# Performance work log

Measured on AMD Instinct MI355X. Metric: run time of the kernel, lower is better.

## Reference

```python
import jax, jax.numpy as jnp
import numpy as np

B, N, D = 4, 2048, 1024


def setup_inputs() -> dict:
    key = jax.random.key(0)
    ks = jax.random.split(key, 9)
    x = jax.random.normal(ks[0], (B, N, D), dtype=jnp.float32)
    # causal mask: True = masked (set to -inf), per dot_product_attention semantics
    mask = jnp.triu(jnp.ones((N, N), dtype=bool), k=1)
    mask = jnp.broadcast_to(mask, (B, N, N))
    scale = 1.0 / np.sqrt(D)
    Wq = jax.random.normal(ks[1], (D, D), dtype=jnp.float32) * scale
    Wk = jax.random.normal(ks[2], (D, D), dtype=jnp.float32) * scale
    Wv = jax.random.normal(ks[3], (D, D), dtype=jnp.float32) * scale
    Wo = jax.random.normal(ks[4], (D, D), dtype=jnp.float32) * scale
    bq = jnp.zeros((D,), dtype=jnp.float32)
    bk = jnp.zeros((D,), dtype=jnp.float32)
    bv = jnp.zeros((D,), dtype=jnp.float32)
    bo = jnp.zeros((D,), dtype=jnp.float32)
    return {"x": x, "mask": mask, "Wq": Wq, "bq": bq, "Wk": Wk, "bk": bk,
            "Wv": Wv, "bv": bv, "Wo": Wo, "bo": bo}


def reference(x, mask, Wq, bq, Wk, bk, Wv, bv, Wo, bo):
    # QKV projections (single-head despite docstring; module never splits heads)
    Q = x @ Wq + bq  # [b, n, d]
    K = x @ Wk + bk
    V = x @ Wv + bv
    d = K.shape[-1]
    scores = jnp.einsum('bqd,bkd->bqk', Q, K) / jnp.sqrt(jnp.asarray(d, Q.dtype))
    min_infty = jnp.finfo(scores.dtype).min
    scores = jnp.where(mask, min_infty, scores)
    weights = jax.nn.softmax(scores, axis=-1)
    attention = jnp.einsum('bqk,bkd->bqd', weights, V)
    out = attention @ Wo + bo
    return out
```

## Files before the change

### kernel.cpp

```cpp
#include <hip/hip_runtime.h>
#include <hip/hip_bf16.h>

typedef __attribute__((ext_vector_type(8))) short short8;
typedef __attribute__((ext_vector_type(4))) float f32x4;

__device__ inline float b2f(unsigned short u) {
    union { unsigned int i; float f; } c; c.i = ((unsigned int)u) << 16; return c.f;
}
__device__ inline unsigned short f2b(float f) {
    __hip_bfloat16 h = __float2bfloat16(f);
    return *reinterpret_cast<unsigned short*>(&h);
}

__device__ inline void gl_lds16(const unsigned short* g, unsigned short* ldsbase) {
    __builtin_amdgcn_global_load_lds(
        (const __attribute__((address_space(1))) unsigned int*)(g),
        (__attribute__((address_space(3))) unsigned int*)(ldsbase),
        16, 0, 0);
}

__global__ __launch_bounds__(256) void prep(
    const float* __restrict__ x,
    const float* __restrict__ Wq, const float* __restrict__ Wk,
    const float* __restrict__ Wo, const float* __restrict__ Wv,
    const float* __restrict__ bv, const float* __restrict__ bo,
    unsigned short* __restrict__ xb,
    unsigned short* __restrict__ Wqt, unsigned short* __restrict__ Wkt,
    unsigned short* __restrict__ Wot, unsigned short* __restrict__ Wvb,
    float* __restrict__ bvo)
{
    const int z = blockIdx.z;
    const int t = threadIdx.x;
    __shared__ float tile[32][33];

    if (z < 3) {
        const float* src = z == 0 ? Wq : z == 1 ? Wk : Wo;
        unsigned short* dst = z == 0 ? Wqt : z == 1 ? Wkt : Wot;
        const int c0 = blockIdx.x * 32, r0 = blockIdx.y * 32;
        const int tx = t & 31, ty = t >> 5;
        #pragma unroll
        for (int i = ty; i < 32; i += 8)
            tile[i][tx] = src[(long)(r0 + i) * 1024 + c0 + tx];
        __syncthreads();
        #pragma unroll
        for (int i = ty; i < 32; i += 8)
            dst[(long)(c0 + i) * 1024 + r0 + tx] = f2b(tile[tx][i]);
        return;
    }
    if (z == 3) {
        const int i = (blockIdx.y * 32 + blockIdx.x) * 256 + t;
        float4 v = ((const float4*)Wv)[i];
        union { unsigned short u[4]; unsigned long long ll; } p;
        p.u[0] = f2b(v.x); p.u[1] = f2b(v.y); p.u[2] = f2b(v.z); p.u[3] = f2b(v.w);
        ((unsigned long long*)Wvb)[i] = p.ll;
        return;
    }
    if (z < 6) {
        const int bl = (z - 4) * 1024 + blockIdx.y * 32 + blockIdx.x;
        #pragma unroll
        for (int k = 0; k < 4; k++) {
            const int i = bl * 1024 + k * 256 + t;
            float4 v = ((const float4*)x)[i];
            union { unsigned short u[4]; unsigned long long ll; } p;
            p.u[0] = f2b(v.x); p.u[1] = f2b(v.y); p.u[2] = f2b(v.z); p.u[3] = f2b(v.w);
            ((unsigned long long*)xb)[i] = p.ll;
        }
        return;
    }
    if (blockIdx.y != 0) return;
    const int tx = t & 31, ty = t >> 5;
    const int n = blockIdx.x * 32 + tx;
    float acc = 0.f;
    #pragma unroll 4
    for (int j = 0; j < 128; j++) {
        const int k = ty * 128 + j;
        acc += Wo[(long)k * 1024 + n] * bv[k];
    }
    float* red = &tile[0][0];
    red[ty * 32 + tx] = acc;
    __syncthreads();
    if (ty == 0) {
        float s = 0.f;
        #pragma unroll
        for (int j = 0; j < 8; j++) s += red[j * 32 + tx];
        bvo[n] = s + bo[n];
    }
}

#define TILE_KLOOP(As, Bs, gA, lda, gB, ldb, Keff) \
    for (int k0 = 0; k0 < (Keff); k0 += 64) { \
        _Pragma("unroll") for (int p = 0; p < 2; p++) \
            _Pragma("unroll") for (int h = 0; h < 2; h++) { \
                gl_lds16((gA) + (long)h * 16 * (lda) + k0 + p * 32, \
                         &(As)[p * 4096 + (w * 32 + h * 16) * 32]); \
                gl_lds16((gB) + (long)h * 16 * (ldb) + k0 + p * 32, \
                         &(Bs)[p * 4096 + (w * 32 + h * 16) * 32]); \
            } \
        __syncthreads(); \
        _Pragma("unroll") for (int p = 0; p < 2; p++) { \
            short8 af[4], bfr[4]; \
            _Pragma("unroll") for (int mi = 0; mi < 4; mi++) \
                af[mi] = *(const short8*)&(As)[p * 4096 + (wr * 64 + mi * 16 + lrow) * 32 + quad * 8]; \
            _Pragma("unroll") for (int ni = 0; ni < 4; ni++) \
                bfr[ni] = *(const short8*)&(Bs)[p * 4096 + (wc * 64 + ni * 16 + lrow) * 32 + quad * 8]; \
            _Pragma("unroll") for (int mi = 0; mi < 4; mi++) \
                _Pragma("unroll") for (int ni = 0; ni < 4; ni++) \
                    acc[mi][ni] = __builtin_amdgcn_mfma_f32_16x16x32_bf16( \
                        af[mi], bfr[ni], acc[mi][ni], 0, 0, 0); \
        } \
        __syncthreads(); \
    }

#define TILE_DECLS \
    const int t = threadIdx.x, lane = t & 63, w = t >> 6; \
    const int wr = w >> 1, wc = w & 1; \
    const int lrow = lane & 15, quad = lane >> 4; \
    f32x4 acc[4][4]; \
    _Pragma("unroll") for (int i = 0; i < 4; i++) \
        _Pragma("unroll") for (int j = 0; j < 4; j++) \
            acc[i][j] = (f32x4){0.f, 0.f, 0.f, 0.f};

__global__ __launch_bounds__(256) void gemm128(
    const unsigned short* __restrict__ A, const unsigned short* __restrict__ Bt,
    unsigned short* __restrict__ C)
{
    __shared__ __attribute__((aligned(16))) unsigned short As[2 * 128 * 32];
    __shared__ __attribute__((aligned(16))) unsigned short Bs[2 * 128 * 32];
    const int m0 = blockIdx.x * 128, n0 = blockIdx.y * 128;

    TILE_DECLS

    const unsigned short* gA = A  + (long)(m0 + w * 32 + (lane >> 2)) * 1024 + (lane & 3) * 8;
    const unsigned short* gB = Bt + (long)(n0 + w * 32 + (lane >> 2)) * 1024 + (lane & 3) * 8;
    TILE_KLOOP(As, Bs, gA, 1024, gB, 1024, 1024)

    #pragma unroll
    for (int mi = 0; mi < 4; mi++) {
        const int m = m0 + wr * 64 + mi * 16 + quad * 4;
        #pragma unroll
        for (int ni = 0; ni < 4; ni++) {
            const int n = n0 + wc * 64 + ni * 16 + lrow;
            #pragma unroll
            for (int rg = 0; rg < 4; rg++)
                C[(long)(m + rg) * 1024 + n] = f2b(acc[mi][ni][rg]);
        }
    }
}

#define TILE2_DECLS \
    const int t = threadIdx.x, lane = t & 63, w = t >> 6; \
    const int wr = w >> 1, wc = w & 1; \
    const int lrow = lane & 15, quad = lane >> 4; \
    f32x4 acc0[4][4], acc1[4][4]; \
    _Pragma("unroll") for (int i = 0; i < 4; i++) \
        _Pragma("unroll") for (int j = 0; j < 4; j++) { \
            acc0[i][j] = (f32x4){0.f, 0.f, 0.f, 0.f}; \
            acc1[i][j] = (f32x4){0.f, 0.f, 0.f, 0.f}; \
        }

#define TILE2_KLOOP(gA, lda, gB0, gB1, ldb, Keff) \
    for (int k0 = 0; k0 < (Keff); k0 += 64) { \
        _Pragma("unroll") for (int p = 0; p < 2; p++) \
            _Pragma("unroll") for (int h = 0; h < 2; h++) { \
                const int ldst = p * 4096 + (w * 32 + h * 16) * 32; \
                const long gofs = (long)h * 16 * (lda) + k0 + p * 32; \
                const long gofsB = (long)h * 16 * (ldb) + k0 + p * 32; \
                gl_lds16((gA)  + gofs,  &As[ldst]); \
                gl_lds16((gB0) + gofsB, &Bs0[ldst]); \
                gl_lds16((gB1) + gofsB, &Bs1[ldst]); \
            } \
        __syncthreads(); \
        _Pragma("unroll") for (int p = 0; p < 2; p++) { \
            short8 af[4], bfr[4]; \
            _Pragma("unroll") for (int mi = 0; mi < 4; mi++) \
                af[mi] = *(const short8*)&As[p * 4096 + (wr * 64 + mi * 16 + lrow) * 32 + quad * 8]; \
            _Pragma("unroll") for (int ni = 0; ni < 4; ni++) \
                bfr[ni] = *(const short8*)&Bs0[p * 4096 + (wc * 64 + ni * 16 + lrow) * 32 + quad * 8]; \
            _Pragma("unroll") for (int mi = 0; mi < 4; mi++) \
                _Pragma("unroll") for (int ni = 0; ni < 4; ni++) \
                    acc0[mi][ni] = __builtin_amdgcn_mfma_f32_16x16x32_bf16( \
                        af[mi], bfr[ni], acc0[mi][ni], 0, 0, 0); \
            _Pragma("unroll") for (int ni = 0; ni < 4; ni++) \
                bfr[ni] = *(const short8*)&Bs1[p * 4096 + (wc * 64 + ni * 16 + lrow) * 32 + quad * 8]; \
            _Pragma("unroll") for (int mi = 0; mi < 4; mi++) \
                _Pragma("unroll") for (int ni = 0; ni < 4; ni++) \
                    acc1[mi][ni] = __builtin_amdgcn_mfma_f32_16x16x32_bf16( \
                        af[mi], bfr[ni], acc1[mi][ni], 0, 0, 0); \
        } \
        __syncthreads(); \
    }

__global__ __launch_bounds__(256, 2) void gemm_qk2(
    const unsigned short* __restrict__ Q, const unsigned short* __restrict__ Km,
    unsigned short* __restrict__ S)
{
    __shared__ __attribute__((aligned(16))) unsigned short As[8192];
    __shared__ __attribute__((aligned(16))) unsigned short Bs0[8192];
    __shared__ __attribute__((aligned(16))) unsigned short Bs1[8192];

    const int q = 71 - blockIdx.x;
    int tq = (int)sqrtf((float)q);
    while (tq * tq + tq > q) tq--;
    while ((tq + 1) * (tq + 1) + (tq + 1) <= q) tq++;
    int bm, bp;
    if (q >= (tq + 1) * (tq + 1)) { bm = 2 * tq + 1; bp = q - (tq + 1) * (tq + 1); }
    else                          { bm = 2 * tq;     bp = q - (tq * tq + tq); }
    const int bz = blockIdx.y;
    const unsigned short* A  = Q  + (long)bz * 2048 * 1024;
    const unsigned short* Bt = Km + (long)bz * 2048 * 1024;
    const int m0 = bm * 128, n0 = bp * 256;

    TILE2_DECLS

    const unsigned short* gA  = A  + (long)(m0 + w * 32 + (lane >> 2)) * 1024 + (lane & 3) * 8;
    const unsigned short* gB0 = Bt + (long)(n0 + w * 32 + (lane >> 2)) * 1024 + (lane & 3) * 8;
    const unsigned short* gB1 = gB0 + 128L * 1024;
    TILE2_KLOOP(gA, 1024, gB0, gB1, 1024, 1024)

    unsigned short* Sb = S + (long)bz * 2048 * 2048;
    #pragma unroll
    for (int mi = 0; mi < 4; mi++) {
        const int m = m0 + wr * 64 + mi * 16 + quad * 4;
        #pragma unroll
        for (int ni = 0; ni < 4; ni++) {
            const int nl = wc * 64 + ni * 16 + lrow;
            #pragma unroll
            for (int rg = 0; rg < 4; rg++) {
                Sb[(long)(m + rg) * 2048 + n0 + nl]       = f2b(acc0[mi][ni][rg] * 0.03125f);
                Sb[(long)(m + rg) * 2048 + n0 + 128 + nl] = f2b(acc1[mi][ni][rg] * 0.03125f);
            }
        }
    }
}

__global__ __launch_bounds__(256, 4) void gemm_pv1(
    const unsigned short* __restrict__ S, const unsigned short* __restrict__ Vot,
    const float* __restrict__ bvo, float* __restrict__ out)
{
    __shared__ __attribute__((aligned(16))) unsigned short As[8192];
    __shared__ __attribute__((aligned(16))) unsigned short Bs[4096];

    const int bn = blockIdx.x;
    const int bm = 15 - (int)blockIdx.y;
    const int bz = blockIdx.z;
    const unsigned short* A  = S   + (long)bz * 2048 * 2048;
    const unsigned short* Bt = Vot + (long)bz * 2048;
    const int m0 = bm * 128, n0 = bn * 64;
    const int Keff = (bm + 1) * 128;

    const int t = threadIdx.x, lane = t & 63, w = t >> 6;
    const int lrow = lane & 15, quad = lane >> 4;

    f32x4 acc[2][4];
    #pragma unroll
    for (int i = 0; i < 2; i++)
        #pragma unroll
        for (int j = 0; j < 4; j++)
            acc[i][j] = (f32x4){0.f, 0.f, 0.f, 0.f};

    const unsigned short* gA = A  + (long)(m0 + w * 32 + (lane >> 2)) * 2048 + (lane & 3) * 8;
    const unsigned short* gB = Bt + (long)(n0 + w * 16 + (lane >> 2)) * 8192 + (lane & 3) * 8;

    for (int k0 = 0; k0 < Keff; k0 += 64) {
        #pragma unroll
        for (int p = 0; p < 2; p++) {
            #pragma unroll
            for (int h = 0; h < 2; h++)
                gl_lds16(gA + (long)h * 16 * 2048 + k0 + p * 32,
                         &As[p * 4096 + (w * 32 + h * 16) * 32]);
            gl_lds16(gB + k0 + p * 32, &Bs[p * 2048 + (w * 16) * 32]);
        }
        __syncthreads();
        #pragma unroll
        for (int p = 0; p < 2; p++) {
            short8 af[2], bfr[4];
            #pragma unroll
            for (int mi = 0; mi < 2; mi++)
                af[mi] = *(const short8*)&As[p * 4096 + (w * 32 + mi * 16 + lrow) * 32 + quad * 8];
            #pragma unroll
            for (int ni = 0; ni < 4; ni++)
                bfr[ni] = *(const short8*)&Bs[p * 2048 + (ni * 16 + lrow) * 32 + quad * 8];
            #pragma unroll
            for (int mi = 0; mi < 2; mi++)
                #pragma unroll
                for (int ni = 0; ni < 4; ni++)
                    acc[mi][ni] = __builtin_amdgcn_mfma_f32_16x16x32_bf16(
                        af[mi], bfr[ni], acc[mi][ni], 0, 0, 0);
        }
        __syncthreads();
    }

    float* ob = out + (long)bz * 2048 * 1024;
    #pragma unroll
    for (int mi = 0; mi < 2; mi++) {
        const int m = m0 + w * 32 + mi * 16 + quad * 4;
        #pragma unroll
        for (int ni = 0; ni < 4; ni++) {
            const int n = n0 + ni * 16 + lrow;
            const float bvl = bvo[n];
            #pragma unroll
            for (int rg = 0; rg < 4; rg++)
                ob[(long)(m + rg) * 1024 + n] = acc[mi][ni][rg] + bvl;
        }
    }
}

__global__ __launch_bounds__(256, 2) void qkv_proj(
    const unsigned short* __restrict__ A,
    const unsigned short* __restrict__ Wqt, const unsigned short* __restrict__ Wkt,
    const unsigned short* __restrict__ Wvot,
    const float* __restrict__ bq, const float* __restrict__ bk,
    unsigned short* __restrict__ Q, unsigned short* __restrict__ Km,
    unsigned short* __restrict__ Vot)
{
    __shared__ __attribute__((aligned(16))) unsigned short smem[32768];
    unsigned short* As  = smem;
    unsigned short* Bs0 = smem + 8192;
    unsigned short* Bs1 = smem + 16384;
    unsigned short* Bs2 = smem + 24576;
    unsigned short* pool = smem;

    const int bid = blockIdx.x;
    const int bnn = bid & 7, bm = bid >> 3;
    const int m0 = bm * 128, n0 = bnn * 128;

    const int t = threadIdx.x, lane = t & 63, w = t >> 6;
    const int wr = w >> 1, wc = w & 1;
    const int lrow = lane & 15, quad = lane >> 4;

    f32x4 accQ[4][4], accK[4][4], accV[4][4];
    #pragma unroll
    for (int i = 0; i < 4; i++)
        #pragma unroll
        for (int j = 0; j < 4; j++) {
            accQ[i][j] = (f32x4){0.f, 0.f, 0.f, 0.f};
            accK[i][j] = (f32x4){0.f, 0.f, 0.f, 0.f};
            accV[i][j] = (f32x4){0.f, 0.f, 0.f, 0.f};
        }

    const long rowA = (long)(m0 + w * 32 + (lane >> 2)) * 1024 + (lane & 3) * 8;
    const long rowB = (long)(n0 + w * 32 + (lane >> 2)) * 1024 + (lane & 3) * 8;
    const unsigned short* gA  = A    + rowA;
    const unsigned short* gB0 = Wqt  + rowB;
    const unsigned short* gB1 = Wkt  + rowB;
    const unsigned short* gB2 = Wvot + rowB;

    for (int k0 = 0; k0 < 1024; k0 += 64) {
        #pragma unroll
        for (int p = 0; p < 2; p++)
            #pragma unroll
            for (int h = 0; h < 2; h++) {
                const int ldst = p * 4096 + (w * 32 + h * 16) * 32;
                const long gofs = (long)h * 16 * 1024 + k0 + p * 32;
                gl_lds16(gA  + gofs, &As[ldst]);
                gl_lds16(gB0 + gofs, &Bs0[ldst]);
                gl_lds16(gB1 + gofs, &Bs1[ldst]);
                gl_lds16(gB2 + gofs, &Bs2[ldst]);
            }
        __syncthreads();
        #pragma unroll
        for (int p = 0; p < 2; p++) {
            short8 af[4], bfr[4];
            #pragma unroll
            for (int mi = 0; mi < 4; mi++)
                af[mi] = *(const short8*)&As[p * 4096 + (wr * 64 + mi * 16 + lrow) * 32 + quad * 8];
            #pragma unroll
            for (int ni = 0; ni < 4; ni++)
                bfr[ni] = *(const short8*)&Bs0[p * 4096 + (wc * 64 + ni * 16 + lrow) * 32 + quad * 8];
            #pragma unroll
            for (int mi = 0; mi < 4; mi++)
                #pragma unroll
                for (int ni = 0; ni < 4; ni++)
                    accQ[mi][ni] = __builtin_amdgcn_mfma_f32_16x16x32_bf16(
                        af[mi], bfr[ni], accQ[mi][ni], 0, 0, 0);
            #pragma unroll
            for (int ni = 0; ni < 4; ni++)
                bfr[ni] = *(const short8*)&Bs1[p * 4096 + (wc * 64 + ni * 16 + lrow) * 32 + quad * 8];
            #pragma unroll
            for (int mi = 0; mi < 4; mi++)
                #pragma unroll
                for (int ni = 0; ni < 4; ni++)
                    accK[mi][ni] = __builtin_amdgcn_mfma_f32_16x16x32_bf16(
                        af[mi], bfr[ni], accK[mi][ni], 0, 0, 0);
            #pragma unroll
            for (int ni = 0; ni < 4; ni++)
                bfr[ni] = *(const short8*)&Bs2[p * 4096 + (wc * 64 + ni * 16 + lrow) * 32 + quad * 8];
            #pragma unroll
            for (int mi = 0; mi < 4; mi++)
                #pragma unroll
                for (int ni = 0; ni < 4; ni++)
                    accV[mi][ni] = __builtin_amdgcn_mfma_f32_16x16x32_bf16(
                        af[mi], bfr[ni], accV[mi][ni], 0, 0, 0);
        }
        __syncthreads();
    }

    #pragma unroll
    for (int mi = 0; mi < 4; mi++)
        #pragma unroll
        for (int ni = 0; ni < 4; ni++) {
            const int n_l = wc * 64 + ni * 16 + lrow;
            const float bvl = bq[n0 + n_l];
            #pragma unroll
            for (int rg = 0; rg < 4; rg++) {
                const int m_l = wr * 64 + mi * 16 + quad * 4 + rg;
                pool[m_l * 128 + n_l] = f2b(accQ[mi][ni][rg] + bvl);
            }
        }
    __syncthreads();
    #pragma unroll
    for (int it = 0; it < 8; it++) {
        const int idx = it * 256 + t;
        const int m_l = idx >> 4, c = idx & 15;
        short8 v = *(const short8*)&pool[m_l * 128 + c * 8];
        *(short8*)&Q[(long)(m0 + m_l) * 1024 + n0 + c * 8] = v;
    }
    __syncthreads();

    #pragma unroll
    for (int mi = 0; mi < 4; mi++)
        #pragma unroll
        for (int ni = 0; ni < 4; ni++) {
            const int n_l = wc * 64 + ni * 16 + lrow;
            const float bvl = bk[n0 + n_l];
            #pragma unroll
            for (int rg = 0; rg < 4; rg++) {
                const int m_l = wr * 64 + mi * 16 + quad * 4 + rg;
                pool[m_l * 128 + n_l] = f2b(accK[mi][ni][rg] + bvl);
            }
        }
    __syncthreads();
    #pragma unroll
    for (int it = 0; it < 8; it++) {
        const int idx = it * 256 + t;
        const int m_l = idx >> 4, c = idx & 15;
        short8 v = *(const short8*)&pool[m_l * 128 + c * 8];
        *(short8*)&Km[(long)(m0 + m_l) * 1024 + n0 + c * 8] = v;
    }
    __syncthreads();

    #pragma unroll
    for (int mi = 0; mi < 4; mi++)
        #pragma unroll
        for (int ni = 0; ni < 4; ni++) {
            const int n_l = wc * 64 + ni * 16 + lrow;
            const int mb = wr * 64 + mi * 16 + quad * 4;
            union { unsigned short u[4]; unsigned long long ll; } pk;
            #pragma unroll
            for (int rg = 0; rg < 4; rg++) pk.u[rg] = f2b(accV[mi][ni][rg]);
            *(unsigned long long*)&pool[n_l * 128 + (mb ^ ((n_l & 15) << 3))] = pk.ll;
        }
    __syncthreads();
    #pragma unroll
    for (int it = 0; it < 8; it++) {
        const int idx = it * 256 + t;
        const int n_l = idx >> 4, c = idx & 15;
        short8 v = *(const short8*)&pool[n_l * 128 + ((c * 8) ^ ((n_l & 15) << 3))];
        *(short8*)&Vot[(long)(n0 + n_l) * 8192 + m0 + c * 8] = v;
    }
}

__global__ __launch_bounds__(256) void softmax_causal(unsigned short* __restrict__ S)
{
    const int i = blockIdx.x;
    const int t = threadIdx.x;
    const int padded = ((i >> 7) + 1) << 7;
    const int j0 = t * 8;
    const bool active = j0 < padded;

    __shared__ float red[4];

    for (int b = 0; b < 4; b++) {
        unsigned short* base = S + ((long)b * 2048 + i) * 2048;

        float v[8];
        if (active) {
            short8 s8 = *(const short8*)(base + j0);
            #pragma unroll
            for (int jj = 0; jj < 8; jj++)
                v[jj] = (j0 + jj <= i) ? b2f((unsigned short)s8[jj]) : -3.0e38f;
        } else {
            #pragma unroll
            for (int jj = 0; jj < 8; jj++) v[jj] = -3.0e38f;
        }

        float lmax = v[0];
        #pragma unroll
        for (int jj = 1; jj < 8; jj++) lmax = fmaxf(lmax, v[jj]);
        #pragma unroll
        for (int off = 32; off > 0; off >>= 1) lmax = fmaxf(lmax, __shfl_xor(lmax, off, 64));
        if ((t & 63) == 0) red[t >> 6] = lmax;
        __syncthreads();
        const float gmax = fmaxf(fmaxf(red[0], red[1]), fmaxf(red[2], red[3]));
        __syncthreads();

        float lsum = 0.f;
        #pragma unroll
        for (int jj = 0; jj < 8; jj++) {
            v[jj] = (v[jj] > -1.0e37f) ? __expf(v[jj] - gmax) : 0.f;
            lsum += v[jj];
        }
        #pragma unroll
        for (int off = 32; off > 0; off >>= 1) lsum += __shfl_xor(lsum, off, 64);
        if ((t & 63) == 0) red[t >> 6] = lsum;
        __syncthreads();
        const float inv = 1.0f / (red[0] + red[1] + red[2] + red[3]);

        if (active) {
            short8 p8;
            #pragma unroll
            for (int jj = 0; jj < 8; jj++) p8[jj] = (short)f2b(v[jj] * inv);
            *(short8*)(base + j0) = p8;
        }
        __syncthreads();
    }
}

extern "C" void kernel_launch(void* const* d_in, const int* in_sizes, int n_in,
                              void* d_out, int out_size, void* d_ws, size_t ws_size,
                              hipStream_t stream)
{
    const float* x  = (const float*)d_in[0];
    const float* Wq = (const float*)d_in[2];
    const float* bq = (const float*)d_in[3];
    const float* Wk = (const float*)d_in[4];
    const float* bk = (const float*)d_in[5];
    const float* Wv = (const float*)d_in[6];
    const float* bv = (const float*)d_in[7];
    const float* Wo = (const float*)d_in[8];
    const float* bo = (const float*)d_in[9];

    unsigned short* ws = (unsigned short*)d_ws;
    const long XSZ = 8192L * 1024;
    const long WSZ = 1024L * 1024;
    unsigned short* xb   = ws;
    unsigned short* Wqt  = ws + XSZ;
    unsigned short* Wkt  = Wqt + WSZ;
    unsigned short* Wot  = Wkt + WSZ;
    unsigned short* Wvb  = Wot + WSZ;
    unsigned short* Wvot = Wvb + WSZ;
    unsigned short* Q    = Wvot + WSZ;
    unsigned short* Km   = Q + XSZ;
    unsigned short* Vot  = Km + XSZ;
    unsigned short* S    = Vot + XSZ;
    float*          bvo  = (float*)(S + 4L * 2048 * 2048);

    const dim3 blk(256);

    prep<<<dim3(32, 32, 7), blk, 0, stream>>>(
        x, Wq, Wk, Wo, Wv, bv, bo, xb, Wqt, Wkt, Wot, Wvb, bvo);

    gemm128<<<dim3(8, 8), blk, 0, stream>>>(Wot, Wvb, Wvot);

    qkv_proj<<<dim3(512), blk, 0, stream>>>(
        xb, Wqt, Wkt, Wvot, bq, bk, Q, Km, Vot);

    gemm_qk2<<<dim3(72, 4), blk, 0, stream>>>(Q, Km, S);

    softmax_causal<<<dim3(2048), blk, 0, stream>>>(S);

    gemm_pv1<<<dim3(16, 16, 4), blk, 0, stream>>>(S, Vot, bvo, (float*)d_out);
}
```

Before: 326.6 us.

## Use deep-K swizzled LDS tiles for Wvo GEMM and XCD-aware PV block mapping

Replaces the small Wo·Wv GEMM with a kernel that stages 256-wide K chunks into large XOR-swizzled LDS tiles. The aim is fewer barriers per K step and fewer LDS bank conflicts. The PV GEMM now runs on a flattened 1D grid remapped so blocks sharing the same batch and row-tile land on the same XCD, for L2 reuse of S, and its occupancy hint goes from 4 to 5. The large LDS footprint limits the Wvo kernel to one block per CU, and the higher hint may add register pressure.

```diff
diff --git a/kernel.cpp b/kernel.cpp
--- a/kernel.cpp
+++ b/kernel.cpp
@@ -87,52 +87,58 @@
     }
 }
 
-#define TILE_KLOOP(As, Bs, gA, lda, gB, ldb, Keff) \
-    for (int k0 = 0; k0 < (Keff); k0 += 64) { \
-        _Pragma("unroll") for (int p = 0; p < 2; p++) \
-            _Pragma("unroll") for (int h = 0; h < 2; h++) { \
-                gl_lds16((gA) + (long)h * 16 * (lda) + k0 + p * 32, \
-                         &(As)[p * 4096 + (w * 32 + h * 16) * 32]); \
-                gl_lds16((gB) + (long)h * 16 * (ldb) + k0 + p * 32, \
-                         &(Bs)[p * 4096 + (w * 32 + h * 16) * 32]); \
-            } \
-        __syncthreads(); \
-        _Pragma("unroll") for (int p = 0; p < 2; p++) { \
-            short8 af[4], bfr[4]; \
-            _Pragma("unroll") for (int mi = 0; mi < 4; mi++) \
-                af[mi] = *(const short8*)&(As)[p * 4096 + (wr * 64 + mi * 16 + lrow) * 32 + quad * 8]; \
-            _Pragma("unroll") for (int ni = 0; ni < 4; ni++) \
-                bfr[ni] = *(const short8*)&(Bs)[p * 4096 + (wc * 64 + ni * 16 + lrow) * 32 + quad * 8]; \
-            _Pragma("unroll") for (int mi = 0; mi < 4; mi++) \
-                _Pragma("unroll") for (int ni = 0; ni < 4; ni++) \
-                    acc[mi][ni] = __builtin_amdgcn_mfma_f32_16x16x32_bf16( \
-                        af[mi], bfr[ni], acc[mi][ni], 0, 0, 0); \
-        } \
-        __syncthreads(); \
-    }
-
-#define TILE_DECLS \
-    const int t = threadIdx.x, lane = t & 63, w = t >> 6; \
-    const int wr = w >> 1, wc = w & 1; \
-    const int lrow = lane & 15, quad = lane >> 4; \
-    f32x4 acc[4][4]; \
-    _Pragma("unroll") for (int i = 0; i < 4; i++) \
-        _Pragma("unroll") for (int j = 0; j < 4; j++) \
+__global__ __launch_bounds__(256, 1) void gemm_wvo(
+    const unsigned short* __restrict__ Wot, const unsigned short* __restrict__ Wvb,
+    unsigned short* __restrict__ Wvot)
+{
+    __shared__ __attribute__((aligned(16))) unsigned short As[128 * 256];
+    __shared__ __attribute__((aligned(16))) unsigned short Bs[128 * 256];
+    const int m0 = blockIdx.x * 128, n0 = blockIdx.y * 128;
+    const int t = threadIdx.x, lane = t & 63, w = t >> 6;
+    const int wr = w >> 1, wc = w & 1;
+    const int lrow = lane & 15, quad = lane >> 4;
+
+    f32x4 acc[4][4];
+    #pragma unroll
+    for (int i = 0; i < 4; i++)
+        #pragma unroll
+        for (int j = 0; j < 4; j++)
             acc[i][j] = (f32x4){0.f, 0.f, 0.f, 0.f};
 
-__global__ __launch_bounds__(256) void gemm128(
-    const unsigned short* __restrict__ A, const unsigned short* __restrict__ Bt,
-    unsigned short* __restrict__ C)
-{
-    __shared__ __attribute__((aligned(16))) unsigned short As[2 * 128 * 32];
-    __shared__ __attribute__((aligned(16))) unsigned short Bs[2 * 128 * 32];
-    const int m0 = blockIdx.x * 128, n0 = blockIdx.y * 128;
-
-    TILE_DECLS
-
-    const unsigned short* gA = A  + (long)(m0 + w * 32 + (lane >> 2)) * 1024 + (lane & 3) * 8;
-    const unsigned short* gB = Bt + (long)(n0 + w * 32 + (lane >> 2)) * 1024 + (lane & 3) * 8;
-    TILE_KLOOP(As, Bs, gA, 1024, gB, 1024, 1024)
+    for (int k0 = 0; k0 < 1024; k0 += 256) {
+        #pragma unroll
+        for (int c = 0; c < 16; c++) {
+            const int id = c * 256 + t;
+            const int row = id >> 5;
+            const int src = (id & 31) ^ (row & 7);
+            gl_lds16(Wot + (long)(m0 + row) * 1024 + k0 + src * 8,
+                     &As[(c * 256 + w * 64) * 8]);
+            gl_lds16(Wvb + (long)(n0 + row) * 1024 + k0 + src * 8,
+                     &Bs[(c * 256 + w * 64) * 8]);
+        }
+        __syncthreads();
+        #pragma unroll
+        for (int kp = 0; kp < 8; kp++) {
+            short8 af[4], bfr[4];
+            #pragma unroll
+            for (int mi = 0; mi < 4; mi++) {
+                const int r = wr * 64 + mi * 16 + lrow;
+                af[mi] = *(const short8*)&As[r * 256 + (((kp * 4 + quad) ^ (r & 7)) << 3)];
+            }
+            #pragma unroll
+            for (int ni = 0; ni < 4; ni++) {
+                const int r = wc * 64 + ni * 16 + lrow;
+                bfr[ni] = *(const short8*)&Bs[r * 256 + (((kp * 4 + quad) ^ (r & 7)) << 3)];
+            }
+            #pragma unroll
+            for (int mi = 0; mi < 4; mi++)
+                #pragma unroll
+                for (int ni = 0; ni < 4; ni++)
+                    acc[mi][ni] = __builtin_amdgcn_mfma_f32_16x16x32_bf16(
+                        af[mi], bfr[ni], acc[mi][ni], 0, 0, 0);
+        }
+        __syncthreads();
+    }
 
     #pragma unroll
     for (int mi = 0; mi < 4; mi++) {
@@ -142,7 +148,7 @@
             const int n = n0 + wc * 64 + ni * 16 + lrow;
             #pragma unroll
             for (int rg = 0; rg < 4; rg++)
-                C[(long)(m + rg) * 1024 + n] = f2b(acc[mi][ni][rg]);
+                Wvot[(long)(m + rg) * 1024 + n] = f2b(acc[mi][ni][rg]);
         }
     }
 }
@@ -233,16 +239,19 @@
     }
 }
 
-__global__ __launch_bounds__(256, 4) void gemm_pv1(
+__global__ __launch_bounds__(256, 5) void gemm_pv1(
     const unsigned short* __restrict__ S, const unsigned short* __restrict__ Vot,
     const float* __restrict__ bvo, float* __restrict__ out)
 {
     __shared__ __attribute__((aligned(16))) unsigned short As[8192];
     __shared__ __attribute__((aligned(16))) unsigned short Bs[4096];
 
-    const int bn = blockIdx.x;
-    const int bm = 15 - (int)blockIdx.y;
-    const int bz = blockIdx.z;
+    const int bid = blockIdx.x;
+    const int xcd = bid & 7, s = bid >> 3;
+    const int bn = s & 15, j = s >> 4;
+    const int rank = j * 8 + xcd;
+    const int bz = rank & 3;
+    const int bm = 15 - (rank >> 2);
     const unsigned short* A  = S   + (long)bz * 2048 * 2048;
     const unsigned short* Bt = Vot + (long)bz * 2048;
     const int m0 = bm * 128, n0 = bn * 64;
@@ -255,8 +264,8 @@
     #pragma unroll
     for (int i = 0; i < 2; i++)
         #pragma unroll
-        for (int j = 0; j < 4; j++)
-            acc[i][j] = (f32x4){0.f, 0.f, 0.f, 0.f};
+        for (int jj = 0; jj < 4; jj++)
+            acc[i][jj] = (f32x4){0.f, 0.f, 0.f, 0.f};
 
     const unsigned short* gA = A  + (long)(m0 + w * 32 + (lane >> 2)) * 2048 + (lane & 3) * 8;
     const unsigned short* gB = Bt + (long)(n0 + w * 16 + (lane >> 2)) * 8192 + (lane & 3) * 8;
@@ -550,7 +559,7 @@
     prep<<<dim3(32, 32, 7), blk, 0, stream>>>(
         x, Wq, Wk, Wo, Wv, bv, bo, xb, Wqt, Wkt, Wot, Wvb, bvo);
 
-    gemm128<<<dim3(8, 8), blk, 0, stream>>>(Wot, Wvb, Wvot);
+    gemm_wvo<<<dim3(8, 8), blk, 0, stream>>>(Wot, Wvb, Wvot);
 
     qkv_proj<<<dim3(512), blk, 0, stream>>>(
         xb, Wqt, Wkt, Wvot, bq, bk, Q, Km, Vot);
@@ -559,5 +568,5 @@
 
     softmax_causal<<<dim3(2048), blk, 0, stream>>>(S);
 
-    gemm_pv1<<<dim3(16, 16, 4), blk, 0, stream>>>(S, Vot, bvo, (float*)d_out);
-}
+    gemm_pv1<<<dim3(1024), blk, 0, stream>>>(S, Vot, bvo, (float*)d_out);
+}
```

Result: faster. 302.9 us (-7.3%).
